# Kernel optimization log

Measured on AMD Instinct MI355X. Metric: run time of the kernel, lower is better.

The kernel has to match this reference:

```python
import jax, jax.numpy as jnp
import numpy as np

B, L, Hp, N, E, Z, GC = 32, 512, 192, 512, 128, 64, 3
TEMP, ALPHA, EPS = 0.5, 0.5, 1e-10


def _reparam(k, mu, var):
    return mu + jax.random.normal(k, mu.shape, mu.dtype) * jnp.exp(0.5 * var)


def setup_inputs() -> dict:
    key = jax.random.key(0)
    ks = jax.random.split(key, 42)
    def W(i, shape):
        return jax.random.normal(ks[i], shape, jnp.float32) * 0.02
    return {
        "batch_x": jax.random.normal(ks[0], (B, L, N), jnp.float32),
        "time_x": jax.random.normal(ks[1], (B, L, 7), jnp.float32),
        "time_W": W(2, (7, E)), "time_b": W(3, (E,)),
        "gate_W": W(4, (L, N)), "gate_b": W(5, (N,)),
        "mu_t_W": W(6, (E, Z)), "mu_t_b": W(7, (Z,)),
        "var_t_W": W(8, (E, Z)), "var_t_b": W(9, (Z,)),
        "ser_W": W(10, (L, E)), "ser_b": W(11, (E,)),
        "mu_h_W": W(12, (E, Z)), "mu_h_b": W(13, (Z,)),
        "var_h_W": W(14, (E, Z)), "var_h_b": W(15, (Z,)),
        "wkey": W(16, (Z, 1)), "wquery": W(17, (Z, 1)),
        "mlp_W": W(18, (GC + 1, 1)), "mlp_b": W(19, (1,)),
        "mu_ht_W": W(20, (E, Z)), "mu_ht_b": W(21, (Z,)),
        "var_ht_W": W(22, (E, Z)), "var_ht_b": W(23, (Z,)),
        "inf_W": W(24, (Z, Z)), "inf_b": W(25, (Z,)),
        "mu_zt_W": W(26, (Z, Z)), "mu_zt_b": W(27, (Z,)),
        "var_zt_W": W(28, (Z, Z)), "var_zt_b": W(29, (Z,)),
        "fW1": W(30, (Z, E)), "fb1": W(31, (E,)),
        "fW2": W(32, (E, Hp)), "fb2": W(33, (Hp,)),
        "rW1": W(34, (Z, E)), "rb1": W(35, (E,)),
        "rW2": W(36, (E, L)), "rb2": W(37, (L,)),
        "is_eval": 1,
    }


def _forward(batch_x, time_x, time_W, time_b, gate_W, gate_b, mu_t_W, mu_t_b,
             var_t_W, var_t_b, ser_W, ser_b, mu_h_W, mu_h_b, var_h_W, var_h_b,
             wkey, wquery, mlp_W, mlp_b, mu_ht_W, mu_ht_b, var_ht_W, var_ht_b,
             inf_W, inf_b, mu_zt_W, mu_zt_b, var_zt_W, var_zt_b,
             fW1, fb1, fW2, fb2, rW1, rb1, rW2, rb2):
    kz1, kz2, kg = jax.random.split(jax.random.key(42), 3)
    # TimeFeatureEmbedding + gate_layer_0 (Linear over the L axis)
    t = time_x @ time_W + time_b                                   # [B,L,E]
    t = jnp.einsum('ble,ln->bne', t, gate_W) + gate_b[None, :, None]  # [B,N,E]
    mu_t = t @ mu_t_W + mu_t_b
    var_t = t @ var_t_W + var_t_b
    # SeriesEmbedding: per-series Linear L->E, fused with time embedding
    h = jnp.einsum('bln,le->bne', batch_x, ser_W) + ser_b          # [B,N,E]
    h_hat = h + t
    mu_h_hat = h_hat @ mu_h_W + mu_h_b
    var_h_hat = h_hat @ var_h_W + var_h_b
    z_hat = _reparam(kz1, mu_h_hat, var_h_hat)                     # [B,N,Z]
    # self_graph_attention: key/query outer-sum -> leakyrelu -> softmax
    ksc = (z_hat @ wkey)[..., 0]                                   # [B,N]
    qsc = (z_hat @ wquery)[..., 0]
    att = jax.nn.softmax(jax.nn.leaky_relu(ksc[:, :, None] + qsc[:, None, :], 0.2), axis=-1)
    # (dropout identity in eval mode)
    lg = (att + 1.0) / 2.0                                         # [B,N,N]
    lg2 = jnp.stack([lg, 1.0 - lg], axis=-1).reshape(N * N, -1)    # [N*N, 2B] (faithful torch reshape)
    g = -jnp.log(-jnp.log(jax.random.uniform(kg, lg2.shape, lg2.dtype) + EPS) + EPS)
    soft = jax.nn.softmax((lg2 + g) / TEMP, axis=-1)
    hard = jax.nn.one_hot(jnp.argmax(soft, axis=-1), soft.shape[-1], dtype=soft.dtype)
    adj = (jax.lax.stop_gradient(hard - soft) + soft)[:, 0].reshape(N, N)
    adj = adj * (1.0 - jnp.eye(N, dtype=adj.dtype))                # masked_fill diagonal
    # graph_convolution: einsum('bnd,nn->bnd') takes the DIAGONAL of adj (faithful)
    diag = jnp.diagonal(adj)
    Hc, outs = h_hat, [h_hat]
    for _ in range(GC):
        Hc = Hc * diag[None, :, None]
        outs.append(Hc)
    h_tilde = (jnp.stack(outs, axis=-1) @ mlp_W + mlp_b)[..., 0]   # [B,N,E]
    mu_ht = h_tilde @ mu_ht_W + mu_ht_b
    var_ht = h_tilde @ var_ht_W + var_ht_b
    z_tilde = _reparam(kz2, mu_ht, var_ht)
    z = ALPHA * z_hat + (1.0 - ALPHA) * z_tilde
    mu_z = ALPHA * mu_h_hat + (1.0 - ALPHA) * mu_ht
    var_z = ALPHA * var_h_hat + (1.0 - ALPHA) * var_ht
    zt = z @ inf_W + inf_b
    mu_zt = zt @ mu_zt_W + mu_zt_b
    var_zt = zt @ var_zt_W + var_zt_b
    y = jnp.transpose((jax.nn.leaky_relu(z @ fW1 + fb1, 0.01) + h) @ fW2 + fb2, (0, 2, 1))  # [B,H,N]
    x = jnp.transpose((jax.nn.leaky_relu(z @ rW1 + rb1, 0.01) + h) @ rW2 + rb2, (0, 2, 1))  # [B,L,N]
    return (x, y, mu_t, var_t, mu_zt, var_zt, mu_z, var_z)


def reference(batch_x, time_x, time_W, time_b, gate_W, gate_b, mu_t_W, mu_t_b,
              var_t_W, var_t_b, ser_W, ser_b, mu_h_W, mu_h_b, var_h_W, var_h_b,
              wkey, wquery, mlp_W, mlp_b, mu_ht_W, mu_ht_b, var_ht_W, var_ht_b,
              inf_W, inf_b, mu_zt_W, mu_zt_b, var_zt_W, var_zt_b,
              fW1, fb1, fW2, fb2, rW1, rb1, rW2, rb2, is_eval):
    # is_eval: both branches of discrete_graph call gumbel_softmax(hard=True)
    return _forward(batch_x, time_x, time_W, time_b, gate_W, gate_b, mu_t_W, mu_t_b,
                    var_t_W, var_t_b, ser_W, ser_b, mu_h_W, mu_h_b, var_h_W, var_h_b,
                    wkey, wquery, mlp_W, mlp_b, mu_ht_W, mu_ht_b, var_ht_W, var_ht_b,
                    inf_W, inf_b, mu_zt_W, mu_zt_b, var_zt_W, var_zt_b,
                    fW1, fb1, fW2, fb2, rW1, rb1, rW2, rb2)
```

## Files before the change

kernel.cpp:

```cpp
#include <hip/hip_runtime.h>
#include <cstdint>
#include <cstddef>

#define B_ 32
#define L_ 512
#define HP_ 192
#define N_ 512
#define E_ 128
#define Z_ 64

typedef short bf16x8 __attribute__((ext_vector_type(8)));
typedef float f32x4 __attribute__((ext_vector_type(4)));

__host__ __device__ __forceinline__ uint32_t rotl32(uint32_t v, int r) {
    return (v << r) | (v >> (32 - r));
}

__host__ __device__ __forceinline__ void tf2x32(uint32_t k0, uint32_t k1,
                                                uint32_t c0, uint32_t c1,
                                                uint32_t& o0, uint32_t& o1) {
    uint32_t ks2 = k0 ^ k1 ^ 0x1BD11BDAu;
    uint32_t x0 = c0 + k0, x1 = c1 + k1;
    x0 += x1; x1 = rotl32(x1, 13); x1 ^= x0;
    x0 += x1; x1 = rotl32(x1, 15); x1 ^= x0;
    x0 += x1; x1 = rotl32(x1, 26); x1 ^= x0;
    x0 += x1; x1 = rotl32(x1, 6);  x1 ^= x0;
    x0 += k1; x1 += ks2 + 1u;
    x0 += x1; x1 = rotl32(x1, 17); x1 ^= x0;
    x0 += x1; x1 = rotl32(x1, 29); x1 ^= x0;
    x0 += x1; x1 = rotl32(x1, 16); x1 ^= x0;
    x0 += x1; x1 = rotl32(x1, 24); x1 ^= x0;
    x0 += ks2; x1 += k0 + 2u;
    x0 += x1; x1 = rotl32(x1, 13); x1 ^= x0;
    x0 += x1; x1 = rotl32(x1, 15); x1 ^= x0;
    x0 += x1; x1 = rotl32(x1, 26); x1 ^= x0;
    x0 += x1; x1 = rotl32(x1, 6);  x1 ^= x0;
    x0 += k0; x1 += k1 + 3u;
    x0 += x1; x1 = rotl32(x1, 17); x1 ^= x0;
    x0 += x1; x1 = rotl32(x1, 29); x1 ^= x0;
    x0 += x1; x1 = rotl32(x1, 16); x1 ^= x0;
    x0 += x1; x1 = rotl32(x1, 24); x1 ^= x0;
    x0 += k1; x1 += ks2 + 4u;
    x0 += x1; x1 = rotl32(x1, 13); x1 ^= x0;
    x0 += x1; x1 = rotl32(x1, 15); x1 ^= x0;
    x0 += x1; x1 = rotl32(x1, 26); x1 ^= x0;
    x0 += x1; x1 = rotl32(x1, 6);  x1 ^= x0;
    x0 += ks2; x1 += k0 + 5u;
    o0 = x0; o1 = x1;
}

__device__ __forceinline__ float erfinv_f(float x) {
    float w = -log1pf(-x * x);
    float p;
    if (w < 5.0f) {
        w = w - 2.5f;
        p = 2.81022636e-08f;
        p = fmaf(p, w, 3.43273939e-07f);
        p = fmaf(p, w, -3.5233877e-06f);
        p = fmaf(p, w, -4.39150654e-06f);
        p = fmaf(p, w, 0.00021858087f);
        p = fmaf(p, w, -0.00125372503f);
        p = fmaf(p, w, -0.00417768164f);
        p = fmaf(p, w, 0.246640727f);
        p = fmaf(p, w, 1.50140941f);
    } else {
        w = sqrtf(w) - 3.0f;
        p = -0.000200214257f;
        p = fmaf(p, w, 0.000100950558f);
        p = fmaf(p, w, 0.00134934322f);
        p = fmaf(p, w, -0.00367342844f);
        p = fmaf(p, w, 0.00573950773f);
        p = fmaf(p, w, -0.0076224613f);
        p = fmaf(p, w, 0.00943887047f);
        p = fmaf(p, w, 1.00167406f);
        p = fmaf(p, w, 2.83297682f);
    }
    return p * x;
}

__device__ __forceinline__ float bits_to_normal(uint32_t bits) {
    float f = __uint_as_float((bits >> 9) | 0x3f800000u) - 1.0f;
    const float lo = -0.99999994f;
    float u = fmaxf(lo, f * 2.0f + lo);
    return 1.41421354f * erfinv_f(u);
}

__device__ __forceinline__ uint32_t f2bf1(float x) {
    uint32_t u = __float_as_uint(x);
    return (u + 0x7fffu + ((u >> 16) & 1u)) >> 16;
}
__device__ __forceinline__ uint32_t f2bf2(float lo, float hi) {
    return f2bf1(lo) | (f2bf1(hi) << 16);
}

#define PO_WT   0
#define PO_WH   16384
#define PO_WI   49152
#define PO_WZZ  53248
#define PO_W1F  61440
#define PO_W1R  69632
#define PO_W2F  77824
#define PO_W2R  102400

struct PrepSrcs { const float* p[13]; };

__global__ void k_prep(PrepSrcs S, short* pool) {
    static const int Kt[13]  = {128,128,128,128,128,128,64,64,64,64,64,128,128};
    static const int Nst[13] = {64,64,64,64,64,64,64,64,64,128,128,192,512};
    static const int Ndt[13] = {128,128,256,256,256,256,64,128,128,128,128,192,512};
    static const int c0t[13] = {0,64,0,64,128,192,0,0,64,0,0,0,0};
    static const int offt[13]= {PO_WT,PO_WT,PO_WH,PO_WH,PO_WH,PO_WH,PO_WI,
                                PO_WZZ,PO_WZZ,PO_W1F,PO_W1R,PO_W2F,PO_W2R};
    int j = blockIdx.y;
    int Ns = Nst[j];
    int total = Kt[j] * Ns;
    int idx = blockIdx.x * 256 + threadIdx.x;
    if (idx >= total) return;
    int k = idx / Ns, nc = idx - k * Ns;
    float v = S.p[j][idx];
    int kc = k >> 5, k32 = k & 31;
    int fg = (k32 >> 2) & 3, e = (k32 & 3) + ((k32 >> 4) << 2);
    pool[offt[j] + (size_t)((kc * 4 + fg) * Ndt[j] + c0t[j] + nc) * 8 + e] = (short)f2bf1(v);
}

__global__ void k_colsum(const float* __restrict__ mW, const float* __restrict__ vW,
                         float* __restrict__ csum) {
    int t = threadIdx.x;
    const float* W = (t < 64) ? mW : vW;
    int zc = t & 63;
    float s = 0.0f;
    for (int e = 0; e < E_; ++e) s += W[e * Z_ + zc];
    csum[t] = s;
}

__global__ __launch_bounds__(256) void k_gate_mfma(
    const float* __restrict__ tx, const float* __restrict__ tW, const float* __restrict__ tb,
    const float* __restrict__ gW, const float* __restrict__ gb,
    const float* __restrict__ bx, const float* __restrict__ sW, const float* __restrict__ sb,
    float* __restrict__ t, float* __restrict__ h, float* __restrict__ hh) {
    __shared__ __align__(16) short sGW[4 * 32 * 8];
    __shared__ __align__(16) short sBX[4 * 32 * 8];
    __shared__ __align__(16) short sT0[4 * 128 * 8];
    __shared__ __align__(16) short sSW[4 * 128 * 8];
    const int b = blockIdx.y, n0 = blockIdx.x * 32;
    const int tid = threadIdx.x;
    const int lane = tid & 63, wave = tid >> 6;
    const int mw = wave & 1, ew = wave >> 1;
    const int aslot = tid & 127, acol = aslot & 31, ag = aslot >> 5, ahalf = tid >> 7;
    const int bg = wave, bcol = (tid & 63) * 2;
    const int fm = lane & 15, fg = lane >> 4;
    const size_t bL = (size_t)b * L_;

    float2 tw[7];
#pragma unroll
    for (int k = 0; k < 7; ++k) tw[k] = *(const float2*)&tW[k * E_ + bcol];
    const float2 tbv = *(const float2*)&tb[bcol];

    const f32x4 zv = {0.f, 0.f, 0.f, 0.f};
    f32x4 accT[4] = {zv, zv, zv, zv};
    f32x4 accH[4] = {zv, zv, zv, zv};

    for (int l0 = 0; l0 < L_; l0 += 32) {
        {
            int lb = l0 + ahalf * 16 + ag * 4;
            float g0 = gW[(size_t)(lb + 0) * N_ + n0 + acol];
            float g1 = gW[(size_t)(lb + 1) * N_ + n0 + acol];
            float g2 = gW[(size_t)(lb + 2) * N_ + n0 + acol];
            float g3 = gW[(size_t)(lb + 3) * N_ + n0 + acol];
            uint2 pg; pg.x = f2bf2(g0, g1); pg.y = f2bf2(g2, g3);
            *(uint2*)&sGW[(ag * 32 + acol) * 8 + ahalf * 4] = pg;
            float x0 = bx[(bL + lb + 0) * N_ + n0 + acol];
            float x1 = bx[(bL + lb + 1) * N_ + n0 + acol];
            float x2 = bx[(bL + lb + 2) * N_ + n0 + acol];
            float x3 = bx[(bL + lb + 3) * N_ + n0 + acol];
            uint2 px; px.x = f2bf2(x0, x1); px.y = f2bf2(x2, x3);
            *(uint2*)&sBX[(ag * 32 + acol) * 8 + ahalf * 4] = px;
        }
        {
            float swA[8], swB[8], tA[8], tB[8];
#pragma unroll
            for (int e = 0; e < 8; ++e) {
                int l = l0 + bg * 4 + (e & 3) + ((e >> 2) << 4);
                float2 wv = *(const float2*)&sW[(size_t)l * E_ + bcol];
                swA[e] = wv.x; swB[e] = wv.y;
                const float* txr = &tx[(bL + l) * 7];
                float a0 = tbv.x, a1 = tbv.y;
#pragma unroll
                for (int k = 0; k < 7; ++k) {
                    float s = txr[k];
                    a0 = fmaf(s, tw[k].x, a0);
                    a1 = fmaf(s, tw[k].y, a1);
                }
                tA[e] = a0; tB[e] = a1;
            }
            uint4 u;
            u.x = f2bf2(swA[0], swA[1]); u.y = f2bf2(swA[2], swA[3]);
            u.z = f2bf2(swA[4], swA[5]); u.w = f2bf2(swA[6], swA[7]);
            *(uint4*)&sSW[(bg * 128 + bcol) * 8] = u;
            u.x = f2bf2(swB[0], swB[1]); u.y = f2bf2(swB[2], swB[3]);
            u.z = f2bf2(swB[4], swB[5]); u.w = f2bf2(swB[6], swB[7]);
            *(uint4*)&sSW[(bg * 128 + bcol + 1) * 8] = u;
            u.x = f2bf2(tA[0], tA[1]); u.y = f2bf2(tA[2], tA[3]);
            u.z = f2bf2(tA[4], tA[5]); u.w = f2bf2(tA[6], tA[7]);
            *(uint4*)&sT0[(bg * 128 + bcol) * 8] = u;
            u.x = f2bf2(tB[0], tB[1]); u.y = f2bf2(tB[2], tB[3]);
            u.z = f2bf2(tB[4], tB[5]); u.w = f2bf2(tB[6], tB[7]);
            *(uint4*)&sT0[(bg * 128 + bcol + 1) * 8] = u;
        }
        __syncthreads();
        bf16x8 fgw = *(const bf16x8*)&sGW[(fg * 32 + mw * 16 + fm) * 8];
        bf16x8 fbx = *(const bf16x8*)&sBX[(fg * 32 + mw * 16 + fm) * 8];
#pragma unroll
        for (int nt = 0; nt < 4; ++nt) {
            int ec = ew * 64 + nt * 16 + fm;
            bf16x8 ft = *(const bf16x8*)&sT0[(fg * 128 + ec) * 8];
            bf16x8 fs = *(const bf16x8*)&sSW[(fg * 128 + ec) * 8];
            accT[nt] = __builtin_amdgcn_mfma_f32_16x16x32_bf16(fgw, ft, accT[nt], 0, 0, 0);
            accH[nt] = __builtin_amdgcn_mfma_f32_16x16x32_bf16(fbx, fs, accH[nt], 0, 0, 0);
        }
        __syncthreads();
    }
    float gbn[4];
#pragma unroll
    for (int r = 0; r < 4; ++r) gbn[r] = gb[n0 + mw * 16 + fg * 4 + r];
#pragma unroll
    for (int nt = 0; nt < 4; ++nt) {
        int e = ew * 64 + nt * 16 + fm;
        float sbe = sb[e];
#pragma unroll
        for (int r = 0; r < 4; ++r) {
            int n = n0 + mw * 16 + fg * 4 + r;
            size_t base = ((size_t)b * N_ + n) * E_ + e;
            float tv = accT[nt][r] + gbn[r];
            float hv = accH[nt][r] + sbe;
            t[base] = tv; h[base] = hv; hh[base] = tv + hv;
        }
    }
}

__global__ __launch_bounds__(256) void k_mega2(
    const float* __restrict__ T, const float* __restrict__ HH,
    const float* __restrict__ h,
    const short* __restrict__ pool,
    const float* __restrict__ bmt_, const float* __restrict__ bvt_,
    const float* __restrict__ bmh, const float* __restrict__ bvh,
    const float* __restrict__ bmht, const float* __restrict__ bvht,
    const float* __restrict__ mlpW, const float* __restrict__ mlpb,
    const float* __restrict__ csum,
    const float* __restrict__ ib,
    const float* __restrict__ mzb, const float* __restrict__ vzb,
    const float* __restrict__ fb1, const float* __restrict__ rb1,
    float* __restrict__ Omt, float* __restrict__ Ovt,
    float* __restrict__ Omz, float* __restrict__ Ovz,
    float* __restrict__ Omzt, float* __restrict__ Ovzt,
    float* __restrict__ tmpF, float* __restrict__ tmpR,
    uint32_t k1a, uint32_t k1b, uint32_t k2a, uint32_t k2b) {
    __shared__ __align__(16) short sAT[4 * 4 * 32 * 8];
    __shared__ __align__(16) short sAH[4 * 4 * 32 * 8];
    __shared__ __align__(16) short sZf[2 * 4 * 32 * 8];
    __shared__ __align__(16) short sZTf[2 * 4 * 32 * 8];
    __shared__ float sOut[32][260];

    const short* Wt  = pool + PO_WT;
    const short* Wh  = pool + PO_WH;
    const short* Wi  = pool + PO_WI;
    const short* Wzz = pool + PO_WZZ;
    const short* W1f = pool + PO_W1F;
    const short* W1r = pool + PO_W1R;

    const int r0 = blockIdx.x * 32;
    const int tid = threadIdx.x;
    const int lane = tid & 63, wv = tid >> 6;
    const int fm = lane & 15, flane = lane >> 4;
    const int m = wv & 1, nb = wv >> 1;
    const f32x4 z4 = {0.f, 0.f, 0.f, 0.f};

#pragma unroll
    for (int it = 0; it < 4; ++it) {
        int idx = tid + it * 256;
        int row = idx >> 5, c4 = idx & 31;
        int k0 = c4 * 4;
        int kc = k0 >> 5, k32 = k0 & 31;
        int fg = (k32 >> 2) & 3, e0 = (k32 >= 16) ? 4 : 0;
        int base = ((kc * 4 + fg) * 32 + row) * 8 + e0;
        float4 v = *(const float4*)&T[(size_t)(r0 + row) * E_ + k0];
        uint2 u; u.x = f2bf2(v.x, v.y); u.y = f2bf2(v.z, v.w);
        *(uint2*)&sAT[base] = u;
        float4 w = *(const float4*)&HH[(size_t)(r0 + row) * E_ + k0];
        uint2 p; p.x = f2bf2(w.x, w.y); p.y = f2bf2(w.z, w.w);
        *(uint2*)&sAH[base] = p;
    }
    __syncthreads();

    {
        bf16x8 fa[4];
#pragma unroll
        for (int kc = 0; kc < 4; ++kc)
            fa[kc] = *(const bf16x8*)&sAT[((kc * 4 + flane) * 32 + m * 16 + fm) * 8];
        f32x4 acc[4] = {z4, z4, z4, z4};
#pragma unroll
        for (int j = 0; j < 4; ++j) {
            int nt = nb + 2 * j;
#pragma unroll
            for (int kc = 0; kc < 4; ++kc) {
                bf16x8 fb = *(const bf16x8*)&Wt[(size_t)((kc * 4 + flane) * 128 + nt * 16 + fm) * 8];
                acc[j] = __builtin_amdgcn_mfma_f32_16x16x32_bf16(fa[kc], fb, acc[j], 0, 0, 0);
            }
        }
#pragma unroll
        for (int j = 0; j < 4; ++j) {
            int ncol = (nb + 2 * j) * 16 + fm;
            float* dst = (ncol < 64) ? Omt : Ovt;
            int zc = ncol & 63;
            float bias = (ncol < 64) ? bmt_[zc] : bvt_[zc];
#pragma unroll
            for (int r = 0; r < 4; ++r) {
                int row = m * 16 + flane * 4 + r;
                dst[(size_t)(r0 + row) * Z_ + zc] = acc[j][r] + bias;
            }
        }
    }

    {
        bf16x8 fa[4];
#pragma unroll
        for (int kc = 0; kc < 4; ++kc)
            fa[kc] = *(const bf16x8*)&sAH[((kc * 4 + flane) * 32 + m * 16 + fm) * 8];
        f32x4 acc[8] = {z4, z4, z4, z4, z4, z4, z4, z4};
#pragma unroll
        for (int j = 0; j < 8; ++j) {
            int nt = nb + 2 * j;
#pragma unroll
            for (int kc = 0; kc < 4; ++kc) {
                bf16x8 fb = *(const bf16x8*)&Wh[(size_t)((kc * 4 + flane) * 256 + nt * 16 + fm) * 8];
                acc[j] = __builtin_amdgcn_mfma_f32_16x16x32_bf16(fa[kc], fb, acc[j], 0, 0, 0);
            }
        }
#pragma unroll
        for (int j = 0; j < 8; ++j) {
            int ncol = (nb + 2 * j) * 16 + fm;
#pragma unroll
            for (int r = 0; r < 4; ++r)
                sOut[m * 16 + flane * 4 + r][ncol] = acc[j][r];
        }
    }
    __syncthreads();

    {
        float w0 = mlpW[0], b0 = mlpb[0];
        int row = tid >> 3;
        int zc0 = (tid & 7) * 8;
        int r = r0 + row;
        float zm[8], zvv[8];
        uint32_t zb[8];
#pragma unroll
        for (int j = 0; j < 8; ++j) {
            int zc = zc0 + j;
            float m1 = sOut[row][zc] + bmh[zc];
            float v1 = sOut[row][64 + zc] + bvh[zc];
            float m2 = fmaf(w0, sOut[row][128 + zc], fmaf(b0, csum[zc], bmht[zc]));
            float v2 = fmaf(w0, sOut[row][192 + zc], fmaf(b0, csum[64 + zc], bvht[zc]));
            uint32_t flat = (uint32_t)r * 64u + (uint32_t)zc;
            uint32_t o0, o1;
            tf2x32(k1a, k1b, 0u, flat, o0, o1);
            float e1 = bits_to_normal(o0 ^ o1);
            tf2x32(k2a, k2b, 0u, flat, o0, o1);
            float e2 = bits_to_normal(o0 ^ o1);
            float zh = m1 + e1 * expf(0.5f * v1);
            float zt = m2 + e2 * expf(0.5f * v2);
            float zval = 0.5f * (zh + zt);
            zb[j] = f2bf1(zval);
            zm[j] = 0.5f * (m1 + m2);
            zvv[j] = 0.5f * (v1 + v2);
        }
        size_t base = (size_t)r * Z_ + zc0;
        *(float4*)&Omz[base]     = make_float4(zm[0], zm[1], zm[2], zm[3]);
        *(float4*)&Omz[base + 4] = make_float4(zm[4], zm[5], zm[6], zm[7]);
        *(float4*)&Ovz[base]     = make_float4(zvv[0], zvv[1], zvv[2], zvv[3]);
        *(float4*)&Ovz[base + 4] = make_float4(zvv[4], zvv[5], zvv[6], zvv[7]);
        int kc = zc0 >> 5, z32 = zc0 & 31;
        int fgA = (z32 >> 2) & 3, eA = (z32 >= 16) ? 4 : 0;
        uint2 u;
        u.x = zb[0] | (zb[1] << 16); u.y = zb[2] | (zb[3] << 16);
        *(uint2*)&sZf[((kc * 4 + fgA) * 32 + row) * 8 + eA] = u;
        u.x = zb[4] | (zb[5] << 16); u.y = zb[6] | (zb[7] << 16);
        *(uint2*)&sZf[((kc * 4 + fgA + 1) * 32 + row) * 8 + eA] = u;
    }
    __syncthreads();

    {
        bf16x8 fa[2];
#pragma unroll
        for (int kc = 0; kc < 2; ++kc)
            fa[kc] = *(const bf16x8*)&sZf[((kc * 4 + flane) * 32 + m * 16 + fm) * 8];
        f32x4 acc[2] = {z4, z4};
#pragma unroll
        for (int j = 0; j < 2; ++j) {
            int nt = nb + 2 * j;
#pragma unroll
            for (int kc = 0; kc < 2; ++kc) {
                bf16x8 fb = *(const bf16x8*)&Wi[(size_t)((kc * 4 + flane) * 64 + nt * 16 + fm) * 8];
                acc[j] = __builtin_amdgcn_mfma_f32_16x16x32_bf16(fa[kc], fb, acc[j], 0, 0, 0);
            }
        }
#pragma unroll
        for (int j = 0; j < 2; ++j) {
            int col = (nb + 2 * j) * 16 + fm;
            float bias = ib[col];
            int kc2 = col >> 5, c32 = col & 31;
            int fg2 = (c32 >> 2) & 3, e2 = (c32 & 3) + ((c32 >> 4) << 2);
#pragma unroll
            for (int r = 0; r < 4; ++r) {
                int row2 = m * 16 + flane * 4 + r;
                sZTf[((kc2 * 4 + fg2) * 32 + row2) * 8 + e2] = (short)f2bf1(acc[j][r] + bias);
            }
        }
    }
    __syncthreads();

    {
        bf16x8 fa[2];
#pragma unroll
        for (int kc = 0; kc < 2; ++kc)
            fa[kc] = *(const bf16x8*)&sZTf[((kc * 4 + flane) * 32 + m * 16 + fm) * 8];
        f32x4 acc[4] = {z4, z4, z4, z4};
#pragma unroll
        for (int j = 0; j < 4; ++j) {
            int nt = nb + 2 * j;
#pragma unroll
            for (int kc = 0; kc < 2; ++kc) {
                bf16x8 fb = *(const bf16x8*)&Wzz[(size_t)((kc * 4 + flane) * 128 + nt * 16 + fm) * 8];
                acc[j] = __builtin_amdgcn_mfma_f32_16x16x32_bf16(fa[kc], fb, acc[j], 0, 0, 0);
            }
        }
#pragma unroll
        for (int j = 0; j < 4; ++j) {
            int ncol = (nb + 2 * j) * 16 + fm;
            float* dst = (ncol < 64) ? Omzt : Ovzt;
            int zc = ncol & 63;
            float bias = (ncol < 64) ? mzb[zc] : vzb[zc];
#pragma unroll
            for (int r = 0; r < 4; ++r) {
                int row = m * 16 + flane * 4 + r;
                dst[(size_t)(r0 + row) * Z_ + zc] = acc[j][r] + bias;
            }
        }
    }

    {
        bf16x8 fa[2];
#pragma unroll
        for (int kc = 0; kc < 2; ++kc)
            fa[kc] = *(const bf16x8*)&sZf[((kc * 4 + flane) * 32 + m * 16 + fm) * 8];
#pragma unroll
        for (int head = 0; head < 2; ++head) {
            const short* W1 = head ? W1r : W1f;
            const float* b1 = head ? rb1 : fb1;
            float* outp = head ? tmpR : tmpF;
            f32x4 acc[4] = {z4, z4, z4, z4};
#pragma unroll
            for (int j = 0; j < 4; ++j) {
                int nt = nb + 2 * j;
#pragma unroll
                for (int kc = 0; kc < 2; ++kc) {
                    bf16x8 fb = *(const bf16x8*)&W1[(size_t)((kc * 4 + flane) * 128 + nt * 16 + fm) * 8];
                    acc[j] = __builtin_amdgcn_mfma_f32_16x16x32_bf16(fa[kc], fb, acc[j], 0, 0, 0);
                }
            }
#pragma unroll
            for (int j = 0; j < 4; ++j) {
                int col = (nb + 2 * j) * 16 + fm;
                float bias = b1[col];
#pragma unroll
                for (int r = 0; r < 4; ++r) {
                    int row = m * 16 + flane * 4 + r;
                    size_t gi = (size_t)(r0 + row) * E_ + col;
                    float v = acc[j][r] + bias;
                    v = (v > 0.0f) ? v : 0.01f * v;
                    outp[gi] = v + h[gi];
                }
            }
        }
    }
}

__global__ __launch_bounds__(256) void k_out_mfma(
    const float* __restrict__ tmp, const short* __restrict__ Wpack,
    const float* __restrict__ b2, float* __restrict__ out, int Dout) {
    __shared__ __align__(16) short sB[4 * 4 * 64 * 8];
    const int r0 = blockIdx.x * 64;
    const int d0 = blockIdx.y * 64;
    const int b = r0 >> 9, nbase = r0 & 511;
    const int tid = threadIdx.x, lane = tid & 63, wave = tid >> 6;
    const int fm = lane & 15, fg = lane >> 4;
    const int col = tid & 63, sg = tid >> 6;
#pragma unroll
    for (int kc = 0; kc < 4; ++kc) {
        float4 b0 = *(const float4*)&tmp[(size_t)(r0 + col) * E_ + kc * 32 + sg * 4];
        float4 b1 = *(const float4*)&tmp[(size_t)(r0 + col) * E_ + kc * 32 + 16 + sg * 4];
        uint4 v;
        v.x = f2bf2(b0.x, b0.y); v.y = f2bf2(b0.z, b0.w);
        v.z = f2bf2(b1.x, b1.y); v.w = f2bf2(b1.z, b1.w);
        *(uint4*)&sB[((kc * 4 + sg) * 64 + col) * 8] = v;
    }
    __syncthreads();
    const f32x4 zv = {0.f, 0.f, 0.f, 0.f};
    f32x4 acc[4] = {zv, zv, zv, zv};
#pragma unroll
    for (int kc = 0; kc < 4; ++kc) {
        bf16x8 fa = *(const bf16x8*)&Wpack[(size_t)((kc * 4 + fg) * Dout + d0 + wave * 16 + fm) * 8];
#pragma unroll
        for (int nt = 0; nt < 4; ++nt) {
            bf16x8 fb = *(const bf16x8*)&sB[((kc * 4 + fg) * 64 + nt * 16 + fm) * 8];
            acc[nt] = __builtin_amdgcn_mfma_f32_16x16x32_bf16(fa, fb, acc[nt], 0, 0, 0);
        }
    }
#pragma unroll
    for (int r = 0; r < 4; ++r) {
        int d = d0 + wave * 16 + fg * 4 + r;
        float bb = b2[d];
#pragma unroll
        for (int nt = 0; nt < 4; ++nt) {
            int n = nbase + nt * 16 + fm;
            out[((size_t)b * Dout + d) * N_ + n] = acc[nt][r] + bb;
        }
    }
}

extern "C" void kernel_launch(void* const* d_in, const int* in_sizes, int n_in,
                              void* d_out, int out_size, void* d_ws, size_t ws_size,
                              hipStream_t stream) {
    (void)in_sizes; (void)n_in; (void)out_size; (void)ws_size;
    const float* batch_x = (const float*)d_in[0];
    const float* time_x  = (const float*)d_in[1];
    const float* time_W  = (const float*)d_in[2];
    const float* time_b  = (const float*)d_in[3];
    const float* gate_W  = (const float*)d_in[4];
    const float* gate_b  = (const float*)d_in[5];
    const float* mu_t_W  = (const float*)d_in[6];
    const float* mu_t_b  = (const float*)d_in[7];
    const float* var_t_W = (const float*)d_in[8];
    const float* var_t_b = (const float*)d_in[9];
    const float* ser_W   = (const float*)d_in[10];
    const float* ser_b   = (const float*)d_in[11];
    const float* mu_h_W  = (const float*)d_in[12];
    const float* mu_h_b  = (const float*)d_in[13];
    const float* var_h_W = (const float*)d_in[14];
    const float* var_h_b = (const float*)d_in[15];
    const float* mlp_W   = (const float*)d_in[18];
    const float* mlp_b   = (const float*)d_in[19];
    const float* mu_ht_W = (const float*)d_in[20];
    const float* mu_ht_b = (const float*)d_in[21];
    const float* var_ht_W = (const float*)d_in[22];
    const float* var_ht_b = (const float*)d_in[23];
    const float* inf_W   = (const float*)d_in[24];
    const float* inf_b   = (const float*)d_in[25];
    const float* mu_zt_W = (const float*)d_in[26];
    const float* mu_zt_b = (const float*)d_in[27];
    const float* var_zt_W = (const float*)d_in[28];
    const float* var_zt_b = (const float*)d_in[29];
    const float* fW1 = (const float*)d_in[30];
    const float* fb1 = (const float*)d_in[31];
    const float* fW2 = (const float*)d_in[32];
    const float* fb2 = (const float*)d_in[33];
    const float* rW1 = (const float*)d_in[34];
    const float* rb1 = (const float*)d_in[35];
    const float* rW2 = (const float*)d_in[36];
    const float* rb2 = (const float*)d_in[37];

    float* out = (float*)d_out;
    float* ws = (float*)d_ws;

    const size_t off_pool = 1048576;
    const size_t off_t    = 2097152;
    const size_t off_tmpF = 2097152;
    const size_t off_h    = 4194304;
    const size_t off_hh   = 6291456;
    const size_t off_tmpR = 6291456;
    const size_t off_csum = 8388608;

    short* pool = (short*)(ws + off_pool);

    float* o_x     = out;
    float* o_y     = out + 8388608;
    float* o_mu_t  = out + 11534336;
    float* o_var_t = out + 12582912;
    float* o_mu_zt = out + 13631488;
    float* o_var_zt= out + 14680064;
    float* o_mu_z  = out + 15728640;
    float* o_var_z = out + 16777216;

    uint32_t kz1a, kz1b, kz2a, kz2b;
    tf2x32(0u, 42u, 0u, 0u, kz1a, kz1b);
    tf2x32(0u, 42u, 0u, 1u, kz2a, kz2b);

    PrepSrcs S;
    S.p[0] = mu_t_W;  S.p[1] = var_t_W;
    S.p[2] = mu_h_W;  S.p[3] = var_h_W; S.p[4] = mu_ht_W; S.p[5] = var_ht_W;
    S.p[6] = inf_W;   S.p[7] = mu_zt_W; S.p[8] = var_zt_W;
    S.p[9] = fW1;     S.p[10] = rW1;    S.p[11] = fW2;    S.p[12] = rW2;

    k_colsum<<<1, 128, 0, stream>>>(mu_ht_W, var_ht_W, ws + off_csum);
    k_prep<<<dim3(256, 13), 256, 0, stream>>>(S, pool);
    k_gate_mfma<<<dim3(16, B_), 256, 0, stream>>>(time_x, time_W, time_b,
                                                  gate_W, gate_b,
                                                  batch_x, ser_W, ser_b,
                                                  ws + off_t, ws + off_h, ws + off_hh);
    k_mega2<<<512, 256, 0, stream>>>(ws + off_t, ws + off_hh, ws + off_h, pool,
                                     mu_t_b, var_t_b, mu_h_b, var_h_b,
                                     mu_ht_b, var_ht_b, mlp_W, mlp_b,
                                     ws + off_csum, inf_b, mu_zt_b, var_zt_b,
                                     fb1, rb1,
                                     o_mu_t, o_var_t, o_mu_z, o_var_z,
                                     o_mu_zt, o_var_zt,
                                     ws + off_tmpF, ws + off_tmpR,
                                     kz1a, kz1b, kz2a, kz2b);
    k_out_mfma<<<dim3(256, HP_ / 64), 256, 0, stream>>>(ws + off_tmpF, pool + PO_W2F,
                                                        fb2, o_y, HP_);
    k_out_mfma<<<dim3(256, L_ / 64), 256, 0, stream>>>(ws + off_tmpR, pool + PO_W2R,
                                                       rb2, o_x, L_);
}
```

Measured before the change: 262.8 us.

## Pre-pack gate operands to bf16 fragment layout and drop LDS staging in gate kernel

Adds a k_pack kernel that converts gate_W, ser_W and the time embedding into bf16 MFMA fragment layout once in global memory, and folds the column-sum kernel into it. The gate kernel is rewritten to read fragments directly from global memory with no shared memory or barriers. It also splits E across a new grid dimension, giving twice as many blocks. This removes redundant per-block recomputation of the time embedding and the repeated conversions of weights, in exchange for an extra launch, extra workspace traffic, and uncoalesced strided batch_x loads.

After: 245.1 us. -6.7%, faster.

```diff
diff --git a/kernel.cpp b/kernel.cpp
--- a/kernel.cpp
+++ b/kernel.cpp
@@ -93,6 +93,8 @@
     return f2bf1(lo) | (f2bf1(hi) << 16);
 }
 
+union U4BF8 { uint4 u; bf16x8 v; };
+
 #define PO_WT   0
 #define PO_WH   16384
 #define PO_WI   49152
@@ -123,114 +125,123 @@
     pool[offt[j] + (size_t)((kc * 4 + fg) * Ndt[j] + c0t[j] + nc) * 8 + e] = (short)f2bf1(v);
 }
 
-__global__ void k_colsum(const float* __restrict__ mW, const float* __restrict__ vW,
-                         float* __restrict__ csum) {
-    int t = threadIdx.x;
-    const float* W = (t < 64) ? mW : vW;
-    int zc = t & 63;
-    float s = 0.0f;
-    for (int e = 0; e < E_; ++e) s += W[e * Z_ + zc];
-    csum[t] = s;
-}
-
-__global__ __launch_bounds__(256) void k_gate_mfma(
-    const float* __restrict__ tx, const float* __restrict__ tW, const float* __restrict__ tb,
-    const float* __restrict__ gW, const float* __restrict__ gb,
-    const float* __restrict__ bx, const float* __restrict__ sW, const float* __restrict__ sb,
+__global__ void k_pack(const float* __restrict__ gW, const float* __restrict__ sW,
+                       const float* __restrict__ tx, const float* __restrict__ tW,
+                       const float* __restrict__ tb,
+                       const float* __restrict__ mW, const float* __restrict__ vW,
+                       short* __restrict__ gfp, short* __restrict__ swp,
+                       short* __restrict__ t0p, float* __restrict__ csum) {
+    int mode = blockIdx.y;
+    int idx = blockIdx.x * 256 + threadIdx.x;
+    if (mode == 0) {
+        if (idx >= 32768) return;
+        int n = idx & 511, r = idx >> 9;
+        int kc = r >> 2, fg = r & 3;
+        int lb = kc * 32 + fg * 4;
+        float v[8];
+#pragma unroll
+        for (int j = 0; j < 8; ++j)
+            v[j] = gW[(size_t)(lb + (j & 3) + ((j >> 2) << 4)) * N_ + n];
+        U4BF8 u;
+        u.u.x = f2bf2(v[0], v[1]); u.u.y = f2bf2(v[2], v[3]);
+        u.u.z = f2bf2(v[4], v[5]); u.u.w = f2bf2(v[6], v[7]);
+        *(uint4*)&gfp[(size_t)((((n >> 5) * 16 + kc) * 4 + fg) * 32 + (n & 31)) * 8] = u.u;
+    } else if (mode == 1) {
+        if (idx >= 8192) return;
+        int e = idx & 127, r = idx >> 7;
+        int kc = r >> 2, fg = r & 3;
+        int lb = kc * 32 + fg * 4;
+        float v[8];
+#pragma unroll
+        for (int j = 0; j < 8; ++j)
+            v[j] = sW[(size_t)(lb + (j & 3) + ((j >> 2) << 4)) * E_ + e];
+        U4BF8 u;
+        u.u.x = f2bf2(v[0], v[1]); u.u.y = f2bf2(v[2], v[3]);
+        u.u.z = f2bf2(v[4], v[5]); u.u.w = f2bf2(v[6], v[7]);
+        *(uint4*)&swp[(size_t)(r * 128 + e) * 8] = u.u;
+    } else if (mode == 2) {
+        if (idx >= 262144) return;
+        int e = idx & 127, r2 = idx >> 7;
+        int b = r2 >> 6, kf = r2 & 63;
+        int kc = kf >> 2, fg = kf & 3;
+        int lb = kc * 32 + fg * 4;
+        float tbe = tb[e];
+        float twc[7];
+#pragma unroll
+        for (int k = 0; k < 7; ++k) twc[k] = tW[k * E_ + e];
+        float v[8];
+#pragma unroll
+        for (int j = 0; j < 8; ++j) {
+            int l = lb + (j & 3) + ((j >> 2) << 4);
+            const float* txr = &tx[((size_t)b * L_ + l) * 7];
+            float a = tbe;
+#pragma unroll
+            for (int k = 0; k < 7; ++k) a = fmaf(txr[k], twc[k], a);
+            v[j] = a;
+        }
+        U4BF8 u;
+        u.u.x = f2bf2(v[0], v[1]); u.u.y = f2bf2(v[2], v[3]);
+        u.u.z = f2bf2(v[4], v[5]); u.u.w = f2bf2(v[6], v[7]);
+        *(uint4*)&t0p[(size_t)(r2 * 128 + e) * 8] = u.u;
+    } else {
+        if (idx >= 128) return;
+        const float* W = (idx < 64) ? mW : vW;
+        int zc = idx & 63;
+        float s = 0.0f;
+        for (int e = 0; e < E_; ++e) s += W[e * Z_ + zc];
+        csum[idx] = s;
+    }
+}
+
+__global__ __launch_bounds__(256) void k_gate4(
+    const float* __restrict__ bx,
+    const short* __restrict__ gfp, const short* __restrict__ swp,
+    const short* __restrict__ t0p,
+    const float* __restrict__ gb, const float* __restrict__ sb,
     float* __restrict__ t, float* __restrict__ h, float* __restrict__ hh) {
-    __shared__ __align__(16) short sGW[4 * 32 * 8];
-    __shared__ __align__(16) short sBX[4 * 32 * 8];
-    __shared__ __align__(16) short sT0[4 * 128 * 8];
-    __shared__ __align__(16) short sSW[4 * 128 * 8];
-    const int b = blockIdx.y, n0 = blockIdx.x * 32;
-    const int tid = threadIdx.x;
-    const int lane = tid & 63, wave = tid >> 6;
-    const int mw = wave & 1, ew = wave >> 1;
-    const int aslot = tid & 127, acol = aslot & 31, ag = aslot >> 5, ahalf = tid >> 7;
-    const int bg = wave, bcol = (tid & 63) * 2;
-    const int fm = lane & 15, fg = lane >> 4;
-    const size_t bL = (size_t)b * L_;
-
-    float2 tw[7];
-#pragma unroll
-    for (int k = 0; k < 7; ++k) tw[k] = *(const float2*)&tW[k * E_ + bcol];
-    const float2 tbv = *(const float2*)&tb[bcol];
-
-    const f32x4 zv = {0.f, 0.f, 0.f, 0.f};
-    f32x4 accT[4] = {zv, zv, zv, zv};
-    f32x4 accH[4] = {zv, zv, zv, zv};
-
-    for (int l0 = 0; l0 < L_; l0 += 32) {
-        {
-            int lb = l0 + ahalf * 16 + ag * 4;
-            float g0 = gW[(size_t)(lb + 0) * N_ + n0 + acol];
-            float g1 = gW[(size_t)(lb + 1) * N_ + n0 + acol];
-            float g2 = gW[(size_t)(lb + 2) * N_ + n0 + acol];
-            float g3 = gW[(size_t)(lb + 3) * N_ + n0 + acol];
-            uint2 pg; pg.x = f2bf2(g0, g1); pg.y = f2bf2(g2, g3);
-            *(uint2*)&sGW[(ag * 32 + acol) * 8 + ahalf * 4] = pg;
-            float x0 = bx[(bL + lb + 0) * N_ + n0 + acol];
-            float x1 = bx[(bL + lb + 1) * N_ + n0 + acol];
-            float x2 = bx[(bL + lb + 2) * N_ + n0 + acol];
-            float x3 = bx[(bL + lb + 3) * N_ + n0 + acol];
-            uint2 px; px.x = f2bf2(x0, x1); px.y = f2bf2(x2, x3);
-            *(uint2*)&sBX[(ag * 32 + acol) * 8 + ahalf * 4] = px;
-        }
-        {
-            float swA[8], swB[8], tA[8], tB[8];
-#pragma unroll
-            for (int e = 0; e < 8; ++e) {
-                int l = l0 + bg * 4 + (e & 3) + ((e >> 2) << 4);
-                float2 wv = *(const float2*)&sW[(size_t)l * E_ + bcol];
-                swA[e] = wv.x; swB[e] = wv.y;
-                const float* txr = &tx[(bL + l) * 7];
-                float a0 = tbv.x, a1 = tbv.y;
-#pragma unroll
-                for (int k = 0; k < 7; ++k) {
-                    float s = txr[k];
-                    a0 = fmaf(s, tw[k].x, a0);
-                    a1 = fmaf(s, tw[k].y, a1);
-                }
-                tA[e] = a0; tB[e] = a1;
-            }
-            uint4 u;
-            u.x = f2bf2(swA[0], swA[1]); u.y = f2bf2(swA[2], swA[3]);
-            u.z = f2bf2(swA[4], swA[5]); u.w = f2bf2(swA[6], swA[7]);
-            *(uint4*)&sSW[(bg * 128 + bcol) * 8] = u;
-            u.x = f2bf2(swB[0], swB[1]); u.y = f2bf2(swB[2], swB[3]);
-            u.z = f2bf2(swB[4], swB[5]); u.w = f2bf2(swB[6], swB[7]);
-            *(uint4*)&sSW[(bg * 128 + bcol + 1) * 8] = u;
-            u.x = f2bf2(tA[0], tA[1]); u.y = f2bf2(tA[2], tA[3]);
-            u.z = f2bf2(tA[4], tA[5]); u.w = f2bf2(tA[6], tA[7]);
-            *(uint4*)&sT0[(bg * 128 + bcol) * 8] = u;
-            u.x = f2bf2(tB[0], tB[1]); u.y = f2bf2(tB[2], tB[3]);
-            u.z = f2bf2(tB[4], tB[5]); u.w = f2bf2(tB[6], tB[7]);
-            *(uint4*)&sT0[(bg * 128 + bcol + 1) * 8] = u;
-        }
-        __syncthreads();
-        bf16x8 fgw = *(const bf16x8*)&sGW[(fg * 32 + mw * 16 + fm) * 8];
-        bf16x8 fbx = *(const bf16x8*)&sBX[(fg * 32 + mw * 16 + fm) * 8];
-#pragma unroll
-        for (int nt = 0; nt < 4; ++nt) {
-            int ec = ew * 64 + nt * 16 + fm;
-            bf16x8 ft = *(const bf16x8*)&sT0[(fg * 128 + ec) * 8];
-            bf16x8 fs = *(const bf16x8*)&sSW[(fg * 128 + ec) * 8];
+    const int ntile = blockIdx.x, eh = blockIdx.y, b = blockIdx.z;
+    const int tid = threadIdx.x, lane = tid & 63, wv = tid >> 6;
+    const int mw = wv & 1, ew = wv >> 1;
+    const int fm = lane & 15, fl = lane >> 4;
+    const int n0 = ntile * 32;
+    const int e0 = eh * 64 + ew * 32;
+    const int n = n0 + mw * 16 + fm;
+    const float* bxp = &bx[(size_t)b * L_ * N_ + n];
+
+    const f32x4 z4 = {0.f, 0.f, 0.f, 0.f};
+    f32x4 accT[2] = {z4, z4}, accH[2] = {z4, z4};
+
+    for (int kc = 0; kc < 16; ++kc) {
+        int lb = kc * 32 + fl * 4;
+        float xv[8];
+#pragma unroll
+        for (int j = 0; j < 8; ++j)
+            xv[j] = bxp[(size_t)(lb + (j & 3) + ((j >> 2) << 4)) * N_];
+        U4BF8 ux;
+        ux.u.x = f2bf2(xv[0], xv[1]); ux.u.y = f2bf2(xv[2], xv[3]);
+        ux.u.z = f2bf2(xv[4], xv[5]); ux.u.w = f2bf2(xv[6], xv[7]);
+        bf16x8 fbx = ux.v;
+        bf16x8 fgw = *(const bf16x8*)&gfp[(size_t)(((ntile * 16 + kc) * 4 + fl) * 32 + mw * 16 + fm) * 8];
+#pragma unroll
+        for (int nt = 0; nt < 2; ++nt) {
+            int ec = e0 + nt * 16 + fm;
+            bf16x8 ft = *(const bf16x8*)&t0p[(size_t)(((b * 16 + kc) * 4 + fl) * 128 + ec) * 8];
+            bf16x8 fs = *(const bf16x8*)&swp[(size_t)((kc * 4 + fl) * 128 + ec) * 8];
             accT[nt] = __builtin_amdgcn_mfma_f32_16x16x32_bf16(fgw, ft, accT[nt], 0, 0, 0);
             accH[nt] = __builtin_amdgcn_mfma_f32_16x16x32_bf16(fbx, fs, accH[nt], 0, 0, 0);
         }
-        __syncthreads();
     }
     float gbn[4];
 #pragma unroll
-    for (int r = 0; r < 4; ++r) gbn[r] = gb[n0 + mw * 16 + fg * 4 + r];
-#pragma unroll
-    for (int nt = 0; nt < 4; ++nt) {
-        int e = ew * 64 + nt * 16 + fm;
+    for (int r = 0; r < 4; ++r) gbn[r] = gb[n0 + mw * 16 + fl * 4 + r];
+#pragma unroll
+    for (int nt = 0; nt < 2; ++nt) {
+        int e = e0 + nt * 16 + fm;
         float sbe = sb[e];
 #pragma unroll
         for (int r = 0; r < 4; ++r) {
-            int n = n0 + mw * 16 + fg * 4 + r;
-            size_t base = ((size_t)b * N_ + n) * E_ + e;
+            int nr = n0 + mw * 16 + fl * 4 + r;
+            size_t base = ((size_t)b * N_ + nr) * E_ + e;
             float tv = accT[nt][r] + gbn[r];
             float hv = accH[nt][r] + sbe;
             t[base] = tv; h[base] = hv; hh[base] = tv + hv;
@@ -571,7 +582,10 @@
     float* out = (float*)d_out;
     float* ws = (float*)d_ws;
 
+    const size_t off_t0p  = 0;
     const size_t off_pool = 1048576;
+    const size_t off_gfp  = 1245184;
+    const size_t off_swp  = 1376256;
     const size_t off_t    = 2097152;
     const size_t off_tmpF = 2097152;
     const size_t off_h    = 4194304;
@@ -580,6 +594,9 @@
     const size_t off_csum = 8388608;
 
     short* pool = (short*)(ws + off_pool);
+    short* gfp  = (short*)(ws + off_gfp);
+    short* swp  = (short*)(ws + off_swp);
+    short* t0p  = (short*)(ws + off_t0p);
 
     float* o_x     = out;
     float* o_y     = out + 8388608;
@@ -600,12 +617,13 @@
     S.p[6] = inf_W;   S.p[7] = mu_zt_W; S.p[8] = var_zt_W;
     S.p[9] = fW1;     S.p[10] = rW1;    S.p[11] = fW2;    S.p[12] = rW2;
 
-    k_colsum<<<1, 128, 0, stream>>>(mu_ht_W, var_ht_W, ws + off_csum);
     k_prep<<<dim3(256, 13), 256, 0, stream>>>(S, pool);
-    k_gate_mfma<<<dim3(16, B_), 256, 0, stream>>>(time_x, time_W, time_b,
-                                                  gate_W, gate_b,
-                                                  batch_x, ser_W, ser_b,
-                                                  ws + off_t, ws + off_h, ws + off_hh);
+    k_pack<<<dim3(1024, 4), 256, 0, stream>>>(gate_W, ser_W, time_x, time_W, time_b,
+                                              mu_ht_W, var_ht_W,
+                                              gfp, swp, t0p, ws + off_csum);
+    k_gate4<<<dim3(16, 2, B_), 256, 0, stream>>>(batch_x, gfp, swp, t0p,
+                                                 gate_b, ser_b,
+                                                 ws + off_t, ws + off_h, ws + off_hh);
     k_mega2<<<512, 256, 0, stream>>>(ws + off_t, ws + off_hh, ws + off_h, pool,
                                      mu_t_b, var_t_b, mu_h_b, var_h_b,
                                      mu_ht_b, var_ht_b, mlp_W, mlp_b,
```
